# Performance work log

Hardware: AMD Instinct MI355X
Metric: run time of the kernel (lower is better)

## Reference

```python
import jax, jax.numpy as jnp
import numpy as np

DIM = 1024
HEADS = 8
DIM_HEAD = 64
INNER = HEADS * DIM_HEAD  # 512
B, N = 4, 2048            # batch, text length
T, M = 8, 64              # num media, tokens per media
EPS = 1e-5


def setup_inputs() -> dict:
    key = jax.random.key(0)
    ks = jax.random.split(key, 8)
    x = jax.random.normal(ks[0], (B, N, DIM), dtype=jnp.float32)
    media = jax.random.normal(ks[1], (B, T, M, DIM), dtype=jnp.float32)
    # t evenly spaced media markers in the text stream -> text_time ramps 0..T
    loc = jnp.zeros((B, N), dtype=bool).at[:, jnp.arange(T) * (N // T)].set(True)
    aug_exist_idx = jax.random.randint(ks[2], (B, T), 0, 2, dtype=jnp.int32)
    ln_gamma = jnp.ones((DIM,), dtype=jnp.float32)
    ln_beta = jnp.zeros((DIM,), dtype=jnp.float32)
    Wq = jax.random.normal(ks[3], (DIM, INNER), dtype=jnp.float32) * 0.02
    Wkv = jax.random.normal(ks[4], (DIM, 2 * INNER), dtype=jnp.float32) * 0.02
    Wo = jax.random.normal(ks[5], (INNER, DIM), dtype=jnp.float32) * 0.02
    return {"x": x, "media": media, "media_locations": loc,
            "aug_exist_idx": aug_exist_idx, "ln_gamma": ln_gamma,
            "ln_beta": ln_beta, "Wq": Wq, "Wkv": Wkv, "Wo": Wo}


def reference(x, media, media_locations, aug_exist_idx, ln_gamma, ln_beta, Wq, Wkv, Wo):
    b, t, m, d = media.shape
    n = x.shape[1]
    scale = DIM_HEAD ** -0.5

    # LayerNorm over last dim
    mu = jnp.mean(x, axis=-1, keepdims=True)
    var = jnp.mean(jnp.square(x - mu), axis=-1, keepdims=True)
    xn = (x - mu) * jax.lax.rsqrt(var + EPS) * ln_gamma + ln_beta

    q = xn @ Wq                                   # [b, n, inner]
    kv = media.reshape(b, t * m, d) @ Wkv         # [b, tm, 2*inner]
    k, v = jnp.split(kv, 2, axis=-1)

    def to_heads(z):
        return z.reshape(b, -1, HEADS, DIM_HEAD).transpose(0, 2, 1, 3)
    q, k, v = to_heads(q) * scale, to_heads(k), to_heads(v)

    sim = jnp.einsum('bhid,bhjd->bhij', q, k)     # [b, h, n, tm]
    neg = -jnp.finfo(sim.dtype).max

    # location mask: text token attends only to its immediately preceding media
    text_time = jnp.cumsum(media_locations.astype(jnp.int32), axis=-1)  # [b, n]
    media_time = jnp.repeat(jnp.arange(t, dtype=jnp.int32) + 1, m)      # [tm]
    loc_mask = text_time[:, None, :, None] == media_time[None, None, None, :]
    sim = jnp.where(loc_mask, sim, neg)

    # existence mask: only attend to media whose aug_exist_idx == 1
    exist = jnp.repeat(aug_exist_idx, m, axis=-1)                       # [b, tm]
    exist_mask = (exist == 1)[:, None, None, :]
    sim = jnp.where(exist_mask, sim, neg)

    sim = sim - jax.lax.stop_gradient(jnp.max(sim, axis=-1, keepdims=True))
    attn = jax.nn.softmax(sim, axis=-1)
    # note: original's attn.masked_fill(...) is out-of-place with discarded result -> no-op

    out = jnp.einsum('bhij,bhjd->bhid', attn, v)  # [b, h, n, dh]
    out = out.transpose(0, 2, 1, 3).reshape(b, n, INNER)
    return out @ Wo
```

## Files before the change

### kernel.cpp

```cpp
#include <hip/hip_runtime.h>

typedef unsigned short u16;
typedef __bf16 bf16x8 __attribute__((ext_vector_type(8)));
typedef float f32x4 __attribute__((ext_vector_type(4)));

__device__ __forceinline__ u16 f2b(float f) {
  unsigned u = __float_as_uint(f);
  u = u + 0x7fffu + ((u >> 16) & 1u);
  return (u16)(u >> 16);
}
__device__ __forceinline__ float b2f(u16 h) {
  return __uint_as_float(((unsigned)h) << 16);
}

__device__ __forceinline__ void gload16(const void* g, void* l) {
  __builtin_amdgcn_global_load_lds((__attribute__((address_space(1))) void*)g,
                                   (__attribute__((address_space(3))) void*)l, 16, 0, 0);
}

struct PrepSmem {
  float tile[32][33];
};

__device__ __forceinline__ void do_ln(const float* __restrict__ x, const float* __restrict__ g,
                                      const float* __restrict__ be, const int* __restrict__ aug,
                                      u16* __restrict__ xn, int blk) {
  const int wave = threadIdx.x >> 6, lane = threadIdx.x & 63;
  const int row = blk * 4 + wave;
  const int brow = row >> 11, irun = (row & 2047) >> 8;
  if (aug[brow * 8 + irun] != 1) return;
  const float4* xr = (const float4*)(x + (size_t)row * 1024);
  float4 v[4];
  float s = 0.f, s2 = 0.f;
#pragma unroll
  for (int j = 0; j < 4; j++) {
    v[j] = xr[j * 64 + lane];
    s += v[j].x + v[j].y + v[j].z + v[j].w;
    s2 += v[j].x * v[j].x + v[j].y * v[j].y + v[j].z * v[j].z + v[j].w * v[j].w;
  }
#pragma unroll
  for (int off = 32; off; off >>= 1) { s += __shfl_xor(s, off); s2 += __shfl_xor(s2, off); }
  const float mu = s * (1.f / 1024.f);
  const float rs = rsqrtf(s2 * (1.f / 1024.f) - mu * mu + 1e-5f);
  ushort4* xo = (ushort4*)(xn + (size_t)row * 1024);
#pragma unroll
  for (int j = 0; j < 4; j++) {
    const float4 gg = ((const float4*)g)[j * 64 + lane];
    const float4 bb = ((const float4*)be)[j * 64 + lane];
    ushort4 o;
    o.x = f2b((v[j].x - mu) * rs * gg.x + bb.x);
    o.y = f2b((v[j].y - mu) * rs * gg.y + bb.y);
    o.z = f2b((v[j].z - mu) * rs * gg.z + bb.z);
    o.w = f2b((v[j].w - mu) * rs * gg.w + bb.w);
    xo[j * 64 + lane] = o;
  }
}

__device__ __forceinline__ void do_transpose(PrepSmem* sm, const float* __restrict__ W,
                                             u16* __restrict__ WT, int K, int N, int bid, int nbx) {
  const int nb = (bid % nbx) * 32, kb = (bid / nbx) * 32;
  const int tx = threadIdx.x & 31, ty = threadIdx.x >> 5;
#pragma unroll
  for (int i = 0; i < 32; i += 8) sm->tile[ty + i][tx] = W[(size_t)(kb + ty + i) * N + nb + tx];
  __syncthreads();
#pragma unroll
  for (int i = 0; i < 32; i += 8) WT[(size_t)(nb + ty + i) * K + kb + tx] = f2b(sm->tile[tx][ty + i]);
}

__device__ __forceinline__ void do_cast(const float* __restrict__ in, u16* __restrict__ out, int blk) {
#pragma unroll
  for (int j = 0; j < 4; j++) {
    const int idx = blk * 1024 + j * 256 + threadIdx.x;
    const float4 v = ((const float4*)in)[idx];
    ushort4 o;
    o.x = f2b(v.x); o.y = f2b(v.y); o.z = f2b(v.z); o.w = f2b(v.w);
    ((ushort4*)out)[idx] = o;
  }
}

__global__ __launch_bounds__(256) void prep_kernel(const float* __restrict__ x,
                                                   const float* __restrict__ gamma,
                                                   const float* __restrict__ beta,
                                                   const float* __restrict__ media,
                                                   const int* __restrict__ aug,
                                                   const float* __restrict__ Wq,
                                                   const float* __restrict__ Wkv,
                                                   const float* __restrict__ Wo,
                                                   u16* __restrict__ xn,
                                                   u16* __restrict__ media_b,
                                                   u16* __restrict__ WqT,
                                                   u16* __restrict__ WkvT,
                                                   u16* __restrict__ WoT,
                                                   float* __restrict__ meanv) {
  __shared__ PrepSmem sm;
  int bid = blockIdx.x;
  if (bid < 2048) { do_ln(x, gamma, beta, aug, xn, bid); return; }
  bid -= 2048;
  if (bid < 512) { do_transpose(&sm, Wq, WqT, 1024, 512, bid, 16); return; }
  bid -= 512;
  if (bid < 1024) { do_transpose(&sm, Wkv, WkvT, 1024, 1024, bid, 32); return; }
  bid -= 1024;
  if (bid < 512) { do_transpose(&sm, Wo, WoT, 512, 1024, bid, 32); return; }
  bid -= 512;
  if (bid < 512) { do_cast(media, media_b, bid); return; }
  bid -= 512;
  meanv[bid * 512 + threadIdx.x] = 0.f;
  meanv[bid * 512 + 256 + threadIdx.x] = 0.f;
}

__device__ __forceinline__ void store_c(float* p, float v) { *p = v; }
__device__ __forceinline__ void store_c(u16* p, float v) { *p = f2b(v); }

template <typename OutT, bool MV>
__device__ __forceinline__ void gemm_body64(const u16* __restrict__ A, const u16* __restrict__ BT,
                                            OutT* __restrict__ C, int N, int K, float alpha,
                                            int row0, int col0, u16* lAs, u16* lBs,
                                            float* __restrict__ meanv) {
  const int tid = threadIdx.x;
  const int wave = tid >> 6;
  const int lane = tid & 63;
  const int lr = lane & 15, lq = lane >> 4;
  const int wm = (wave & 1) * 32, wn = (wave >> 1) * 64;

  const int trow = tid >> 2;
  const int tcol = (tid & 3) * 8;
  const u16* ga = A + (size_t)(row0 + trow) * K + tcol;
  const u16* gb = BT + (size_t)(col0 + trow) * K + tcol;
  char* lA0 = (char*)lAs + wave * 1024;
  char* lB0 = (char*)lBs + wave * 1024;

  f32x4 acc[2][4] = {};

  for (int k0 = 0; k0 < K; k0 += 32) {
    gload16(ga + k0, lA0);
    gload16(gb + k0, lB0);
    gload16(gb + k0 + (size_t)64 * K, lB0 + 4096);
    __syncthreads();
    bf16x8 af[2], bg[4];
#pragma unroll
    for (int mt = 0; mt < 2; mt++)
      af[mt] = *(const bf16x8*)&lAs[(wm + mt * 16 + lr) * 32 + lq * 8];
#pragma unroll
    for (int nt = 0; nt < 4; nt++)
      bg[nt] = *(const bf16x8*)&lBs[(wn + nt * 16 + lr) * 32 + lq * 8];
#pragma unroll
    for (int mt = 0; mt < 2; mt++)
#pragma unroll
      for (int nt = 0; nt < 4; nt++)
        acc[mt][nt] = __builtin_amdgcn_mfma_f32_16x16x32_bf16(af[mt], bg[nt], acc[mt][nt], 0, 0, 0);
    __syncthreads();
  }

#pragma unroll
  for (int mt = 0; mt < 2; mt++) {
#pragma unroll
    for (int nt = 0; nt < 4; nt++) {
      const int r = row0 + wm + mt * 16 + lq * 4;
      const int cc = col0 + wn + nt * 16 + lr;
#pragma unroll
      for (int i = 0; i < 4; i++) {
        store_c(&C[(size_t)(r + i) * N + cc], acc[mt][nt][i] * alpha);
      }
    }
  }

  if constexpr (MV) {
    if (col0 >= 512) {
      const int bmv = row0 >> 9;
#pragma unroll
      for (int nt = 0; nt < 4; nt++) {
        float ps = 0.f;
#pragma unroll
        for (int mt = 0; mt < 2; mt++)
#pragma unroll
          for (int i = 0; i < 4; i++) ps += acc[mt][nt][i];
        ps += __shfl_xor(ps, 16);
        ps += __shfl_xor(ps, 32);
        if (lq == 0) atomicAdd(&meanv[bmv * 512 + (col0 - 512) + wn + nt * 16 + lr], ps);
      }
    }
  }
}

__global__ __launch_bounds__(256) void kv_gemm(const u16* __restrict__ mediab,
                                               const u16* __restrict__ WkvT,
                                               u16* __restrict__ kvb,
                                               float* __restrict__ meanv) {
  __shared__ __align__(16) u16 lAs[64 * 32];
  __shared__ __align__(16) u16 lBs[128 * 32];
  const int bid = blockIdx.x;
  gemm_body64<u16, true>(mediab, WkvT, kvb, 1024, 1024, 1.0f, (bid >> 3) * 64, (bid & 7) * 128,
                         lAs, lBs, meanv);
}

__global__ __launch_bounds__(256) void fattn_kernel(const u16* __restrict__ xn,
                                                    const u16* __restrict__ WqT,
                                                    const u16* __restrict__ kv,
                                                    const float* __restrict__ meanv,
                                                    const u16* __restrict__ WoT,
                                                    const int* __restrict__ aug,
                                                    u16* __restrict__ out,
                                                    float* __restrict__ fbrow) {
  const int bid = blockIdx.x;
  const int tid = threadIdx.x;

  if (bid >= 1024) {
    __shared__ float smv[512];
    const int blk = bid - 1024;
    const int b = blk >> 2, n0 = (blk & 3) * 256;
    smv[tid] = meanv[b * 512 + tid] * (1.f / 512.f);
    smv[tid + 256] = meanv[b * 512 + 256 + tid] * (1.f / 512.f);
    __syncthreads();
    const int n = n0 + tid;
    const u16* wr = WoT + (size_t)n * 512;
    float acc = 0.f;
#pragma unroll 4
    for (int k = 0; k < 512; k += 8) {
      const uint4 w = *(const uint4*)(wr + k);
      acc += smv[k + 0] * __uint_as_float(w.x << 16);
      acc += smv[k + 1] * __uint_as_float(w.x & 0xffff0000u);
      acc += smv[k + 2] * __uint_as_float(w.y << 16);
      acc += smv[k + 3] * __uint_as_float(w.y & 0xffff0000u);
      acc += smv[k + 4] * __uint_as_float(w.z << 16);
      acc += smv[k + 5] * __uint_as_float(w.z & 0xffff0000u);
      acc += smv[k + 6] * __uint_as_float(w.w << 16);
      acc += smv[k + 7] * __uint_as_float(w.w & 0xffff0000u);
    }
    fbrow[b * 1024 + n] = acc;
    return;
  }

  const int b = bid >> 8, h = (bid >> 5) & 7;
  const int q0 = (bid & 31) * 64;
  const int run = q0 >> 8;
  if (aug[b * 8 + run] != 1) return;

  const int c = run;
  const int wave = tid >> 6, lane = tid & 63;
  const int lr = lane & 15, lq = lane >> 4;

  __shared__ __align__(16) u16 lQ[64 * 72];
  __shared__ __align__(16) u16 lK[64 * 72];
  __shared__ __align__(16) u16 lVT[64 * 72];
  __shared__ __align__(16) u16 lP[4][16 * 72];

  {
    u16* lAs = lK;
    u16* lBs = lK + 2048;
    const int trow = tid >> 2, tcol = (tid & 3) * 8;
    const u16* ga = xn + ((size_t)(b * 2048 + q0 + trow)) * 1024 + tcol;
    const u16* gb = WqT + ((size_t)(h * 64 + trow)) * 1024 + tcol;
    char* lA0 = (char*)lAs + wave * 1024;
    char* lB0 = (char*)lBs + wave * 1024;
    f32x4 qa[4] = {};
    for (int k0 = 0; k0 < 1024; k0 += 32) {
      gload16(ga + k0, lA0);
      gload16(gb + k0, lB0);
      __syncthreads();
      const bf16x8 aq = *(const bf16x8*)&lAs[(wave * 16 + lr) * 32 + lq * 8];
      bf16x8 bg[4];
#pragma unroll
      for (int nt = 0; nt < 4; nt++)
        bg[nt] = *(const bf16x8*)&lBs[(nt * 16 + lr) * 32 + lq * 8];
#pragma unroll
      for (int nt = 0; nt < 4; nt++)
        qa[nt] = __builtin_amdgcn_mfma_f32_16x16x32_bf16(aq, bg[nt], qa[nt], 0, 0, 0);
      __syncthreads();
    }
#pragma unroll
    for (int nt = 0; nt < 4; nt++)
#pragma unroll
      for (int i = 0; i < 4; i++)
        lQ[(wave * 16 + lq * 4 + i) * 72 + nt * 16 + lr] = f2b(qa[nt][i] * 0.125f);
  }

  const int srow = tid >> 2, seg = tid & 3;
  {
    const uint4* ksrc = (const uint4*)(kv + ((size_t)(b * 512 + c * 64 + srow)) * 1024 + h * 64 + seg * 16);
    *(uint4*)&lK[srow * 72 + seg * 16] = ksrc[0];
    *(uint4*)&lK[srow * 72 + seg * 16 + 8] = ksrc[1];
    union { uint4 u4[2]; u16 s[16]; } vv;
    const uint4* vsrc = (const uint4*)(kv + ((size_t)(b * 512 + c * 64 + srow)) * 1024 + 512 + h * 64 + seg * 16);
    vv.u4[0] = vsrc[0];
    vv.u4[1] = vsrc[1];
#pragma unroll
    for (int j = 0; j < 16; j++) lVT[(seg * 16 + j) * 72 + srow] = vv.s[j];
  }
  __syncthreads();

  bf16x8 af[2];
#pragma unroll
  for (int ks = 0; ks < 2; ks++)
    af[ks] = *(const bf16x8*)&lQ[(wave * 16 + lr) * 72 + ks * 32 + lq * 8];

  u16* lPw = lP[wave];

  bf16x8 kf[4][2];
#pragma unroll
  for (int nt = 0; nt < 4; nt++)
#pragma unroll
    for (int ks = 0; ks < 2; ks++)
      kf[nt][ks] = *(const bf16x8*)&lK[(nt * 16 + lr) * 72 + ks * 32 + lq * 8];
  f32x4 s[4] = {};
#pragma unroll
  for (int nt = 0; nt < 4; nt++)
#pragma unroll
    for (int ks = 0; ks < 2; ks++)
      s[nt] = __builtin_amdgcn_mfma_f32_16x16x32_bf16(af[ks], kf[nt][ks], s[nt], 0, 0, 0);

  float linv[4];
#pragma unroll
  for (int i = 0; i < 4; i++) {
    float mx = s[0][i];
#pragma unroll
    for (int nt = 1; nt < 4; nt++) mx = fmaxf(mx, s[nt][i]);
    mx = fmaxf(mx, __shfl_xor(mx, 1));
    mx = fmaxf(mx, __shfl_xor(mx, 2));
    mx = fmaxf(mx, __shfl_xor(mx, 4));
    mx = fmaxf(mx, __shfl_xor(mx, 8));
    float rs = 0.f;
#pragma unroll
    for (int nt = 0; nt < 4; nt++) {
      const float pv = __expf(s[nt][i] - mx);
      const u16 pb = f2b(pv);
      lPw[(lq * 4 + i) * 72 + nt * 16 + lr] = pb;
      rs += b2f(pb);
    }
    rs += __shfl_xor(rs, 1);
    rs += __shfl_xor(rs, 2);
    rs += __shfl_xor(rs, 4);
    rs += __shfl_xor(rs, 8);
    linv[i] = 1.0f / rs;
  }
  asm volatile("s_waitcnt lgkmcnt(0)" ::: "memory");

  bf16x8 pa[2];
#pragma unroll
  for (int ks = 0; ks < 2; ks++)
    pa[ks] = *(const bf16x8*)&lPw[lr * 72 + ks * 32 + lq * 8];
  f32x4 o[4] = {};
#pragma unroll
  for (int nt = 0; nt < 4; nt++) {
#pragma unroll
    for (int ks = 0; ks < 2; ks++) {
      const bf16x8 vf = *(const bf16x8*)&lVT[(nt * 16 + lr) * 72 + ks * 32 + lq * 8];
      o[nt] = __builtin_amdgcn_mfma_f32_16x16x32_bf16(pa[ks], vf, o[nt], 0, 0, 0);
    }
  }

#pragma unroll
  for (int i = 0; i < 4; i++) {
    const int qrow = q0 + wave * 16 + lq * 4 + i;
#pragma unroll
    for (int nt = 0; nt < 4; nt++)
      out[((size_t)(b * 2048 + qrow)) * 512 + h * 64 + nt * 16 + lr] = f2b(o[nt][i] * linv[i]);
  }
}

__global__ __launch_bounds__(256) void gemm_out(const u16* __restrict__ A,
                                                const u16* __restrict__ BT,
                                                float* __restrict__ C,
                                                const int* __restrict__ aug,
                                                const float* __restrict__ fbrow) {
  __shared__ __align__(16) u16 lAs[64 * 32];
  __shared__ __align__(16) u16 lBs[128 * 32];
  const int bid = blockIdx.x;
  const int row0 = (bid >> 3) * 64, col0 = (bid & 7) * 128;
  const int b = row0 >> 11, run = (row0 & 2047) >> 8;
  if (aug[b * 8 + run] != 1) {
    const float4 fv = *(const float4*)(fbrow + b * 1024 + col0 + (threadIdx.x & 31) * 4);
#pragma unroll
    for (int pass = 0; pass < 8; pass++) {
      const int r = pass * 8 + (threadIdx.x >> 5);
      *(float4*)(C + (size_t)(row0 + r) * 1024 + col0 + (threadIdx.x & 31) * 4) = fv;
    }
    return;
  }
  gemm_body64<float, false>(A, BT, C, 1024, 512, 1.0f, row0, col0, lAs, lBs, nullptr);
}

extern "C" void kernel_launch(void* const* d_in, const int* in_sizes, int n_in,
                              void* d_out, int out_size, void* d_ws, size_t ws_size,
                              hipStream_t stream) {
  (void)in_sizes; (void)n_in; (void)out_size; (void)ws_size;
  const float* x     = (const float*)d_in[0];
  const float* media = (const float*)d_in[1];
  const int*   aug   = (const int*)d_in[3];
  const float* gamma = (const float*)d_in[4];
  const float* beta  = (const float*)d_in[5];
  const float* Wq    = (const float*)d_in[6];
  const float* Wkv   = (const float*)d_in[7];
  const float* Wo    = (const float*)d_in[8];
  float* out = (float*)d_out;

  char* p = (char*)d_ws;
  u16*   xn      = (u16*)(p + 0);
  u16*   attnout = (u16*)(p + (16u << 20));
  u16*   kvb     = (u16*)(p + (24u << 20));
  u16*   media_b = (u16*)(p + (28u << 20));
  u16*   WqT     = (u16*)(p + (32u << 20));
  u16*   WkvT    = (u16*)(p + (33u << 20));
  u16*   WoT     = (u16*)(p + (35u << 20));
  float* meanv   = (float*)(p + (36u << 20));
  float* fbrow   = (float*)(p + (36u << 20) + (32u << 10));

  prep_kernel<<<dim3(4612), 256, 0, stream>>>(x, gamma, beta, media, aug, Wq, Wkv, Wo,
                                              xn, media_b, WqT, WkvT, WoT, meanv);
  kv_gemm<<<dim3(256), 256, 0, stream>>>(media_b, WkvT, kvb, meanv);
  fattn_kernel<<<dim3(1040), 256, 0, stream>>>(xn, WqT, kvb, meanv, WoT, aug, attnout, fbrow);
  gemm_out<<<dim3(1024), 256, 0, stream>>>(attnout, WoT, out, aug, fbrow);
}
```

Baseline: 157.3 us.

## Fuse KV GEMM into prep kernel reading fp32 media and Wkv directly

Removes the separate kv_gemm launch, along with the media bf16 cast and the Wkv transpose. A new block type in the prep kernel loads fp32 media and Wkv straight from global memory and converts them to bf16 in registers. It then writes them into LDS in MFMA layout. The meanv zeroing moves to a hipMemsetAsync. The fused GEMM loses the async global_load_lds path and uses synchronous float4 loads with strided Wkv row reads. Its 256 blocks run last in the grid, so they may become a tail.

```diff
diff --git a/kernel.cpp b/kernel.cpp
--- a/kernel.cpp
+++ b/kernel.cpp
@@ -67,55 +67,124 @@
   for (int i = 0; i < 32; i += 8) WT[(size_t)(nb + ty + i) * K + kb + tx] = f2b(sm->tile[tx][ty + i]);
 }
 
-__device__ __forceinline__ void do_cast(const float* __restrict__ in, u16* __restrict__ out, int blk) {
-#pragma unroll
-  for (int j = 0; j < 4; j++) {
-    const int idx = blk * 1024 + j * 256 + threadIdx.x;
-    const float4 v = ((const float4*)in)[idx];
-    ushort4 o;
-    o.x = f2b(v.x); o.y = f2b(v.y); o.z = f2b(v.z); o.w = f2b(v.w);
-    ((ushort4*)out)[idx] = o;
-  }
-}
-
-__global__ __launch_bounds__(256) void prep_kernel(const float* __restrict__ x,
-                                                   const float* __restrict__ gamma,
-                                                   const float* __restrict__ beta,
-                                                   const float* __restrict__ media,
-                                                   const int* __restrict__ aug,
-                                                   const float* __restrict__ Wq,
-                                                   const float* __restrict__ Wkv,
-                                                   const float* __restrict__ Wo,
-                                                   u16* __restrict__ xn,
-                                                   u16* __restrict__ media_b,
-                                                   u16* __restrict__ WqT,
-                                                   u16* __restrict__ WkvT,
-                                                   u16* __restrict__ WoT,
-                                                   float* __restrict__ meanv) {
-  __shared__ PrepSmem sm;
+__device__ __forceinline__ void kv_raw_block(const float* __restrict__ media,
+                                             const float* __restrict__ Wkv,
+                                             u16* __restrict__ kvb,
+                                             float* __restrict__ meanv,
+                                             int bid, char* smem) {
+  u16* lAs = (u16*)smem;
+  u16* lBs = (u16*)(smem + 4096);
+  const int tid = threadIdx.x;
+  const int wave = tid >> 6, lane = tid & 63;
+  const int lr = lane & 15, lq = lane >> 4;
+  const int wm = (wave & 1) * 32, wn = (wave >> 1) * 64;
+  const int row0 = (bid >> 3) * 64, col0 = (bid & 7) * 128;
+
+  const int arow = tid >> 2, ak8 = (tid & 3) * 8;
+  const int kp2 = (tid >> 4) * 2, bn8 = (tid & 15) * 8;
+
+  const float* gA = media + (size_t)(row0 + arow) * 1024 + ak8;
+  const float* gB0 = Wkv + (size_t)kp2 * 1024 + col0 + bn8;
+  const float* gB1 = gB0 + 1024;
+
+  f32x4 acc[2][4] = {};
+
+  for (int k0 = 0; k0 < 1024; k0 += 32) {
+    const float4 a0 = *(const float4*)(gA + k0);
+    const float4 a1 = *(const float4*)(gA + k0 + 4);
+    const float4 b00 = *(const float4*)(gB0 + (size_t)k0 * 1024);
+    const float4 b01 = *(const float4*)(gB0 + (size_t)k0 * 1024 + 4);
+    const float4 b10 = *(const float4*)(gB1 + (size_t)k0 * 1024);
+    const float4 b11 = *(const float4*)(gB1 + (size_t)k0 * 1024 + 4);
+
+    unsigned* wa = (unsigned*)&lAs[arow * 32 + ak8];
+    wa[0] = (unsigned)f2b(a0.x) | ((unsigned)f2b(a0.y) << 16);
+    wa[1] = (unsigned)f2b(a0.z) | ((unsigned)f2b(a0.w) << 16);
+    wa[2] = (unsigned)f2b(a1.x) | ((unsigned)f2b(a1.y) << 16);
+    wa[3] = (unsigned)f2b(a1.z) | ((unsigned)f2b(a1.w) << 16);
+
+    const float e0[8] = {b00.x, b00.y, b00.z, b00.w, b01.x, b01.y, b01.z, b01.w};
+    const float e1[8] = {b10.x, b10.y, b10.z, b10.w, b11.x, b11.y, b11.z, b11.w};
+#pragma unroll
+    for (int j = 0; j < 8; j++)
+      *(unsigned*)&lBs[(bn8 + j) * 32 + kp2] =
+          (unsigned)f2b(e0[j]) | ((unsigned)f2b(e1[j]) << 16);
+    __syncthreads();
+
+    bf16x8 af[2], bg[4];
+#pragma unroll
+    for (int mt = 0; mt < 2; mt++)
+      af[mt] = *(const bf16x8*)&lAs[(wm + mt * 16 + lr) * 32 + lq * 8];
+#pragma unroll
+    for (int nt = 0; nt < 4; nt++)
+      bg[nt] = *(const bf16x8*)&lBs[(wn + nt * 16 + lr) * 32 + lq * 8];
+#pragma unroll
+    for (int mt = 0; mt < 2; mt++)
+#pragma unroll
+      for (int nt = 0; nt < 4; nt++)
+        acc[mt][nt] = __builtin_amdgcn_mfma_f32_16x16x32_bf16(af[mt], bg[nt], acc[mt][nt], 0, 0, 0);
+    __syncthreads();
+  }
+
+#pragma unroll
+  for (int mt = 0; mt < 2; mt++) {
+#pragma unroll
+    for (int nt = 0; nt < 4; nt++) {
+      const int r = row0 + wm + mt * 16 + lq * 4;
+      const int cc = col0 + wn + nt * 16 + lr;
+#pragma unroll
+      for (int i = 0; i < 4; i++)
+        kvb[(size_t)(r + i) * 1024 + cc] = f2b(acc[mt][nt][i]);
+    }
+  }
+
+  if (col0 >= 512) {
+    const int bmv = row0 >> 9;
+#pragma unroll
+    for (int nt = 0; nt < 4; nt++) {
+      float ps = 0.f;
+#pragma unroll
+      for (int mt = 0; mt < 2; mt++)
+#pragma unroll
+        for (int i = 0; i < 4; i++) ps += acc[mt][nt][i];
+      ps += __shfl_xor(ps, 16);
+      ps += __shfl_xor(ps, 32);
+      if (lq == 0) atomicAdd(&meanv[bmv * 512 + (col0 - 512) + wn + nt * 16 + lr], ps);
+    }
+  }
+}
+
+__global__ __launch_bounds__(256) void bigprep_kernel(const float* __restrict__ x,
+                                                      const float* __restrict__ gamma,
+                                                      const float* __restrict__ beta,
+                                                      const float* __restrict__ media,
+                                                      const int* __restrict__ aug,
+                                                      const float* __restrict__ Wq,
+                                                      const float* __restrict__ Wkv,
+                                                      const float* __restrict__ Wo,
+                                                      u16* __restrict__ xn,
+                                                      u16* __restrict__ WqT,
+                                                      u16* __restrict__ WoT,
+                                                      u16* __restrict__ kvb,
+                                                      float* __restrict__ meanv) {
+  __shared__ __align__(16) char psm[12288];
   int bid = blockIdx.x;
   if (bid < 2048) { do_ln(x, gamma, beta, aug, xn, bid); return; }
   bid -= 2048;
-  if (bid < 512) { do_transpose(&sm, Wq, WqT, 1024, 512, bid, 16); return; }
+  if (bid < 512) { do_transpose((PrepSmem*)psm, Wq, WqT, 1024, 512, bid, 16); return; }
   bid -= 512;
-  if (bid < 1024) { do_transpose(&sm, Wkv, WkvT, 1024, 1024, bid, 32); return; }
-  bid -= 1024;
-  if (bid < 512) { do_transpose(&sm, Wo, WoT, 512, 1024, bid, 32); return; }
+  if (bid < 512) { do_transpose((PrepSmem*)psm, Wo, WoT, 512, 1024, bid, 32); return; }
   bid -= 512;
-  if (bid < 512) { do_cast(media, media_b, bid); return; }
-  bid -= 512;
-  meanv[bid * 512 + threadIdx.x] = 0.f;
-  meanv[bid * 512 + 256 + threadIdx.x] = 0.f;
+  kv_raw_block(media, Wkv, kvb, meanv, bid, psm);
 }
 
 __device__ __forceinline__ void store_c(float* p, float v) { *p = v; }
 __device__ __forceinline__ void store_c(u16* p, float v) { *p = f2b(v); }
 
-template <typename OutT, bool MV>
+template <typename OutT>
 __device__ __forceinline__ void gemm_body64(const u16* __restrict__ A, const u16* __restrict__ BT,
                                             OutT* __restrict__ C, int N, int K, float alpha,
-                                            int row0, int col0, u16* lAs, u16* lBs,
-                                            float* __restrict__ meanv) {
+                                            int row0, int col0, u16* lAs, u16* lBs) {
   const int tid = threadIdx.x;
   const int wave = tid >> 6;
   const int lane = tid & 63;
@@ -163,34 +232,6 @@
       }
     }
   }
-
-  if constexpr (MV) {
-    if (col0 >= 512) {
-      const int bmv = row0 >> 9;
-#pragma unroll
-      for (int nt = 0; nt < 4; nt++) {
-        float ps = 0.f;
-#pragma unroll
-        for (int mt = 0; mt < 2; mt++)
-#pragma unroll
-          for (int i = 0; i < 4; i++) ps += acc[mt][nt][i];
-        ps += __shfl_xor(ps, 16);
-        ps += __shfl_xor(ps, 32);
-        if (lq == 0) atomicAdd(&meanv[bmv * 512 + (col0 - 512) + wn + nt * 16 + lr], ps);
-      }
-    }
-  }
-}
-
-__global__ __launch_bounds__(256) void kv_gemm(const u16* __restrict__ mediab,
-                                               const u16* __restrict__ WkvT,
-                                               u16* __restrict__ kvb,
-                                               float* __restrict__ meanv) {
-  __shared__ __align__(16) u16 lAs[64 * 32];
-  __shared__ __align__(16) u16 lBs[128 * 32];
-  const int bid = blockIdx.x;
-  gemm_body64<u16, true>(mediab, WkvT, kvb, 1024, 1024, 1.0f, (bid >> 3) * 64, (bid & 7) * 128,
-                         lAs, lBs, meanv);
 }
 
 __global__ __launch_bounds__(256) void fattn_kernel(const u16* __restrict__ xn,
@@ -376,7 +417,7 @@
     }
     return;
   }
-  gemm_body64<float, false>(A, BT, C, 1024, 512, 1.0f, row0, col0, lAs, lBs, nullptr);
+  gemm_body64<float>(A, BT, C, 1024, 512, 1.0f, row0, col0, lAs, lBs);
 }
 
 extern "C" void kernel_launch(void* const* d_in, const int* in_sizes, int n_in,
@@ -397,16 +438,15 @@
   u16*   xn      = (u16*)(p + 0);
   u16*   attnout = (u16*)(p + (16u << 20));
   u16*   kvb     = (u16*)(p + (24u << 20));
-  u16*   media_b = (u16*)(p + (28u << 20));
   u16*   WqT     = (u16*)(p + (32u << 20));
-  u16*   WkvT    = (u16*)(p + (33u << 20));
   u16*   WoT     = (u16*)(p + (35u << 20));
   float* meanv   = (float*)(p + (36u << 20));
   float* fbrow   = (float*)(p + (36u << 20) + (32u << 10));
 
-  prep_kernel<<<dim3(4612), 256, 0, stream>>>(x, gamma, beta, media, aug, Wq, Wkv, Wo,
-                                              xn, media_b, WqT, WkvT, WoT, meanv);
-  kv_gemm<<<dim3(256), 256, 0, stream>>>(media_b, WkvT, kvb, meanv);
+  hipMemsetAsync(meanv, 0, 4 * 512 * sizeof(float), stream);
+
+  bigprep_kernel<<<dim3(3328), 256, 0, stream>>>(x, gamma, beta, media, aug, Wq, Wkv, Wo,
+                                                 xn, WqT, WoT, kvb, meanv);
   fattn_kernel<<<dim3(1040), 256, 0, stream>>>(xn, WqT, kvb, meanv, WoT, aug, attnout, fbrow);
   gemm_out<<<dim3(1024), 256, 0, stream>>>(attnout, WoT, out, aug, fbrow);
 }
```

After: 202.5 us. +28.8%, slower.
